# Performance work log

Hardware: AMD Instinct MI355X
Metric: run time of the kernel (lower is better)

Reference implementation:

```python
import jax, jax.numpy as jnp
import numpy as np

B, C, H, W = 4, 128, 64, 64


def setup_inputs() -> dict:
    key = jax.random.key(0)
    ks = jax.random.split(key, 7)
    s = 1.0 / np.sqrt(C)
    return {
        "x": jax.random.normal(ks[0], (B, C, H, W), dtype=jnp.float32),
        "Wq": jax.random.normal(ks[1], (C, C), dtype=jnp.float32) * s,
        "bq": jnp.zeros((C,), dtype=jnp.float32),
        "Wk": jax.random.normal(ks[2], (C, C), dtype=jnp.float32) * s,
        "bk": jnp.zeros((C,), dtype=jnp.float32),
        "Wv": jax.random.normal(ks[3], (C, C), dtype=jnp.float32) * s,
        "bv": jnp.zeros((C,), dtype=jnp.float32),
    }


def reference(x, Wq, bq, Wk, bk, Wv, bv):
    b, c, h, w = x.shape
    n = h * w
    scale = c ** (-0.5)
    # tokens: [B, N, C]
    xt = x.reshape(b, c, n).transpose(0, 2, 1)
    # 1x1 convs == per-token channel GEMMs (out[c'] = sum_c W[c',c] x[c] + b[c'])
    q = jnp.einsum("bnc,dc->bnd", xt, Wq) + bq  # [B, N, C]
    k = jnp.einsum("bnc,dc->bnd", xt, Wk) + bk  # [B, N, C]
    v = jnp.einsum("bnc,dc->bnd", xt, Wv) + bv  # [B, N, C]
    scores = jnp.einsum("bic,bjc->bij", q, k) * scale  # [B, N, N]
    attn = jax.nn.softmax(scores, axis=-1)
    out = jnp.einsum("bij,bjc->bic", attn, v)  # [B, N, C]
    return out.transpose(0, 2, 1).reshape(b, c, h, w)
```

## Files before the change

### kernel.cpp

```cpp
#include <hip/hip_runtime.h>
#include <hip/hip_bf16.h>


#define BATCH 4
#define CH    128
#define NTOK  4096
#define TK    64
#define SCALE 0.08838834764831845f
#define LOG2E 1.4426950408889634f
#define MFIX  16.0f

typedef __attribute__((ext_vector_type(8)))  short short8;
typedef __attribute__((ext_vector_type(4)))  float f32x4;
typedef __attribute__((ext_vector_type(16))) float f32x16;

static __device__ __forceinline__ unsigned short f2bf(float f) {
    __hip_bfloat16 h = (__hip_bfloat16)f;
    return *(const unsigned short*)&h;
}

static __device__ __forceinline__ unsigned cvt_pk_bf16(float lo, float hi) {
    unsigned r;
    asm("v_cvt_pk_bf16_f32 %0, %1, %2" : "=v"(r) : "v"(lo), "v"(hi));
    return r;
}

__global__ __launch_bounds__(256) void convert_w_kernel(
    const float* __restrict__ Wq, const float* __restrict__ Wk,
    const float* __restrict__ Wv, unsigned short* __restrict__ wb)
{
    const int idx = (blockIdx.x * 256 + threadIdx.x) * 4;
    const float* srcs[3] = {Wq, Wk, Wv};
    #pragma unroll
    for (int m = 0; m < 3; ++m) {
        float4 v = *(const float4*)(srcs[m] + idx);
        unsigned short o[4] = {f2bf(v.x), f2bf(v.y), f2bf(v.z), f2bf(v.w)};
        *(uint2*)(wb + (size_t)m * CH * CH + idx) = *(const uint2*)o;
    }
}

__global__ __launch_bounds__(256) void proj_mfma_kernel(
    const float* __restrict__ x,
    const unsigned short* __restrict__ wb_all,
    const float* __restrict__ bq, const float* __restrict__ bk,
    const float* __restrict__ bv,
    unsigned short* __restrict__ q_ws, unsigned short* __restrict__ k_ws,
    unsigned short* __restrict__ vt_ws)
{
    __shared__ __align__(16) unsigned short XsT[64 * CH];

    const int t    = threadIdx.x;
    const int w    = t >> 6;
    const int lane = t & 63;
    const int quad = lane >> 4;
    const int c16  = lane & 15;
    const int n0   = blockIdx.x * 64;
    const int b    = blockIdx.y;
    const int z    = blockIdx.z;
    const float* xb = x + (size_t)b * CH * NTOK;

    {
        const int tok = lane;
        #pragma unroll
        for (int cc = 0; cc < 4; ++cc) {
            const int cb = 32 * w + 8 * cc;
            unsigned short tmp[8];
            #pragma unroll
            for (int j = 0; j < 8; ++j)
                tmp[j] = f2bf(xb[(size_t)(cb + j) * NTOK + n0 + tok]);
            const int phys = ((cb >> 3) ^ (tok & 15));
            *(short8*)&XsT[tok * CH + phys * 8] = *(const short8*)tmp;
        }
    }
    __syncthreads();

    if (z < 2) {
        const unsigned short* wm = wb_all + (size_t)z * CH * CH;
        const float* bias = (z == 0) ? bq : bk;
        unsigned short* dst = (z == 0) ? q_ws : k_ws;
        const float mul = (z == 0) ? (SCALE * LOG2E) : 1.0f;

        short8 xa[4];
        #pragma unroll
        for (int ks = 0; ks < 4; ++ks)
            xa[ks] = *(const short8*)&XsT[(16 * w + c16) * CH + (((4 * ks + quad) ^ c16) << 3)];

        #pragma unroll
        for (int nt = 0; nt < 8; ++nt) {
            f32x4 a = (f32x4){0.f, 0.f, 0.f, 0.f};
            const unsigned short* wr = wm + (16 * nt + c16) * CH;
            #pragma unroll
            for (int ks = 0; ks < 4; ++ks) {
                const short8 bf = *(const short8*)(wr + 32 * ks + 8 * quad);
                a = __builtin_amdgcn_mfma_f32_16x16x32_bf16(xa[ks], bf, a, 0, 0, 0);
            }
            const float bvv = bias[16 * nt + c16];
            #pragma unroll
            for (int r = 0; r < 4; ++r) {
                const int n = n0 + 16 * w + quad * 4 + r;
                dst[((size_t)b * NTOK + n) * CH + 16 * nt + c16] =
                    f2bf((a[r] + bvv) * mul);
            }
        }
    } else {
        const unsigned short* wvb = wb_all + (size_t)2 * CH * CH;
        short8 wva[2][4];
        float  bvv[2][4];
        #pragma unroll
        for (int mt = 0; mt < 2; ++mt) {
            const int crow16 = 16 * (2 * w + mt);
            #pragma unroll
            for (int ks = 0; ks < 4; ++ks)
                wva[mt][ks] = *(const short8*)&wvb[(crow16 + c16) * CH + 32 * ks + 8 * quad];
            #pragma unroll
            for (int r = 0; r < 4; ++r)
                bvv[mt][r] = bv[crow16 + quad * 4 + r];
        }
        #pragma unroll
        for (int nt = 0; nt < 4; ++nt) {
            short8 xbf[4];
            #pragma unroll
            for (int ks = 0; ks < 4; ++ks)
                xbf[ks] = *(const short8*)&XsT[(16 * nt + c16) * CH + (((4 * ks + quad) ^ c16) << 3)];
            #pragma unroll
            for (int mt = 0; mt < 2; ++mt) {
                f32x4 acc = (f32x4){0.f, 0.f, 0.f, 0.f};
                #pragma unroll
                for (int ks = 0; ks < 4; ++ks)
                    acc = __builtin_amdgcn_mfma_f32_16x16x32_bf16(wva[mt][ks], xbf[ks], acc, 0, 0, 0);
                #pragma unroll
                for (int r = 0; r < 4; ++r) {
                    const int crow = 16 * (2 * w + mt) + quad * 4 + r;
                    vt_ws[((size_t)b * CH + crow) * NTOK + n0 + 16 * nt + c16] =
                        f2bf(acc[r] + bvv[mt][r]);
                }
            }
        }
    }
}

template <int SPLIT>
__global__ __launch_bounds__(256, 2) void flash_attn_mfma(
    const unsigned short* __restrict__ q_ws,
    const unsigned short* __restrict__ k_ws,
    const unsigned short* __restrict__ vt_ws,
    float* __restrict__ out,
    float* __restrict__ Op, float* __restrict__ l_p)
{
    __shared__ __align__(16) unsigned short KsU[2][TK * CH];
    __shared__ __align__(16) unsigned short VtU[2][CH * TK];

    const int t    = threadIdx.x;
    const int w    = t >> 6;
    const int lane = t & 63;
    const int half = lane >> 5;
    const int l32  = lane & 31;
    const int jc   = blockIdx.y;
    const int b    = blockIdx.z;
    const int n0   = blockIdx.x * 128;
    const int jbeg = jc * (NTOK / SPLIT);
    constexpr int NT = (NTOK / SPLIT) / TK;

    const unsigned short* kg = k_ws  + (size_t)b * NTOK * CH;
    const unsigned short* vg = vt_ws + (size_t)b * CH * NTOK;

    short8 qa[8];
    {
        const unsigned short* qrow =
            q_ws + ((size_t)b * NTOK + n0 + 32 * w + l32) * CH;
        #pragma unroll
        for (int ks = 0; ks < 8; ++ks)
            qa[ks] = *(const short8*)(qrow + ks * 16 + half * 8);
    }

    f32x16 Oa[4];
    #pragma unroll
    for (int ct = 0; ct < 4; ++ct) Oa[ct] = (f32x16)(0.0f);
    float lsum = 0.f;

    const int krl = lane >> 4, ku = lane & 15;
    const int vcl = lane >> 3, vu = lane & 7;

    auto STAGE = [&](int buf, int jj) {
        #pragma unroll
        for (int ci = 0; ci < 4; ++ci) {
            const int row = 16 * w + 4 * ci + krl;
            const int g   = ku ^ (row & 15);
            const unsigned short* src = kg + (size_t)(jj + row) * CH + g * 8;
            __builtin_amdgcn_global_load_lds(
                (const __attribute__((address_space(1))) void*)src,
                (__attribute__((address_space(3))) void*)&KsU[buf][(16 * w + 4 * ci) * CH],
                16, 0, 0);
        }
        #pragma unroll
        for (int ci = 0; ci < 4; ++ci) {
            const int c = 32 * w + 8 * ci + vcl;
            const int g = vu ^ (c & 7);
            const unsigned short* src = vg + (size_t)c * NTOK + jj + g * 8;
            __builtin_amdgcn_global_load_lds(
                (const __attribute__((address_space(1))) void*)src,
                (__attribute__((address_space(3))) void*)&VtU[buf][(32 * w + 8 * ci) * TK],
                16, 0, 0);
        }
    };

    STAGE(0, jbeg);

    int j0 = jbeg;
    for (int tt = 0; tt < NT; ++tt, j0 += TK) {
        const int cur = tt & 1;
        if (tt + 1 < NT) {
            STAGE(cur ^ 1, j0 + TK);
            asm volatile("s_waitcnt vmcnt(8)" ::: "memory");
        } else {
            asm volatile("s_waitcnt vmcnt(0)" ::: "memory");
        }
        __builtin_amdgcn_sched_barrier(0);
        __builtin_amdgcn_s_barrier();
        __builtin_amdgcn_sched_barrier(0);

        const unsigned short* Kc = &KsU[cur][0];
        const unsigned short* Vc = &VtU[cur][0];

        f32x16 s[2];
        s[0] = (f32x16)(-MFIX);
        s[1] = (f32x16)(-MFIX);
        #pragma unroll
        for (int ks = 0; ks < 8; ++ks) {
            const int ph = (2 * ks + half) ^ (l32 & 15);
            const short8 kf0 = *(const short8*)&Kc[l32 * CH + ph * 8];
            const short8 kf1 = *(const short8*)&Kc[(32 + l32) * CH + ph * 8];
            s[0] = __builtin_amdgcn_mfma_f32_32x32x16_bf16(kf0, qa[ks], s[0], 0, 0, 0);
            s[1] = __builtin_amdgcn_mfma_f32_32x32x16_bf16(kf1, qa[ks], s[1], 0, 0, 0);
        }

        short8 pb[4];
        #pragma unroll
        for (int kt = 0; kt < 2; ++kt) {
            float p[16];
            #pragma unroll
            for (int r = 0; r < 16; ++r) p[r] = exp2f(s[kt][r]);
            float a0 = 0.f, a1 = 0.f, a2 = 0.f, a3 = 0.f;
            #pragma unroll
            for (int r = 0; r < 4; ++r) {
                a0 += p[r]; a1 += p[4 + r]; a2 += p[8 + r]; a3 += p[12 + r];
            }
            lsum += (a0 + a1) + (a2 + a3);
            unsigned wd[8];
            #pragma unroll
            for (int i = 0; i < 8; ++i) wd[i] = cvt_pk_bf16(p[2 * i], p[2 * i + 1]);
            auto r02 = __builtin_amdgcn_permlane32_swap(wd[0], wd[2], false, false);
            auto r13 = __builtin_amdgcn_permlane32_swap(wd[1], wd[3], false, false);
            auto r46 = __builtin_amdgcn_permlane32_swap(wd[4], wd[6], false, false);
            auto r57 = __builtin_amdgcn_permlane32_swap(wd[5], wd[7], false, false);
            union { unsigned u[4]; short8 s8; } f0, f1;
            f0.u[0] = r02[0]; f0.u[1] = r13[0]; f0.u[2] = r02[1]; f0.u[3] = r13[1];
            f1.u[0] = r46[0]; f1.u[1] = r57[0]; f1.u[2] = r46[1]; f1.u[3] = r57[1];
            pb[2 * kt + 0] = f0.s8;
            pb[2 * kt + 1] = f1.s8;
        }

        #pragma unroll
        for (int ks2 = 0; ks2 < 4; ++ks2) {
            #pragma unroll
            for (int ct = 0; ct < 4; ++ct) {
                const int ch = 32 * ct + l32;
                const int ph = (2 * ks2 + half) ^ (ch & 7);
                const short8 vf = *(const short8*)&Vc[ch * TK + ph * 8];
                Oa[ct] = __builtin_amdgcn_mfma_f32_32x32x16_bf16(vf, pb[ks2], Oa[ct], 0, 0, 0);
            }
        }
        __builtin_amdgcn_sched_barrier(0);
        __builtin_amdgcn_s_barrier();
        __builtin_amdgcn_sched_barrier(0);
    }

    const float lt = lsum + __shfl_xor(lsum, 32);
    const int n = n0 + 32 * w + l32;

    if constexpr (SPLIT == 1) {
        const float inv = 1.0f / lt;
        #pragma unroll
        for (int ct = 0; ct < 4; ++ct) {
            #pragma unroll
            for (int r = 0; r < 16; ++r) {
                const int c = 32 * ct + (r & 3) + 8 * (r >> 2) + 4 * half;
                out[((size_t)b * CH + c) * NTOK + n] = Oa[ct][r] * inv;
            }
        }
    } else {
        const size_t chunk = (size_t)(b * SPLIT + jc);
        #pragma unroll
        for (int ct = 0; ct < 4; ++ct) {
            #pragma unroll
            for (int r = 0; r < 16; ++r) {
                const int c = 32 * ct + (r & 3) + 8 * (r >> 2) + 4 * half;
                Op[(chunk * CH + c) * NTOK + n] = Oa[ct][r];
            }
        }
        if (half == 0) l_p[chunk * NTOK + n] = lt;
    }
}

template <int SPLIT>
__global__ __launch_bounds__(256) void combine_kernel(
    const float* __restrict__ Op, const float* __restrict__ l_p,
    float* __restrict__ out)
{
    const int b = blockIdx.y;
    const size_t idx = ((size_t)blockIdx.x * 256 + threadIdx.x) * 4;
    const int c = (int)(idx >> 12);
    const int n = (int)(idx & (NTOK - 1));
    float4 acc = make_float4(0.f, 0.f, 0.f, 0.f);
    float4 den = make_float4(0.f, 0.f, 0.f, 0.f);
    #pragma unroll
    for (int j = 0; j < SPLIT; ++j) {
        const size_t chunk = (size_t)(b * SPLIT + j);
        const float4 o = *(const float4*)&Op[(chunk * CH + c) * NTOK + n];
        const float4 d = *(const float4*)&l_p[chunk * NTOK + n];
        acc.x += o.x; acc.y += o.y; acc.z += o.z; acc.w += o.w;
        den.x += d.x; den.y += d.y; den.z += d.z; den.w += d.w;
    }
    float4 r;
    r.x = acc.x / den.x; r.y = acc.y / den.y;
    r.z = acc.z / den.z; r.w = acc.w / den.w;
    *(float4*)&out[((size_t)b * CH * NTOK) + idx] = r;
}

extern "C" void kernel_launch(void* const* d_in, const int* in_sizes, int n_in,
                              void* d_out, int out_size, void* d_ws, size_t ws_size,
                              hipStream_t stream) {
    const float* x  = (const float*)d_in[0];
    const float* Wq = (const float*)d_in[1];
    const float* bq = (const float*)d_in[2];
    const float* Wk = (const float*)d_in[3];
    const float* bk = (const float*)d_in[4];
    const float* Wv = (const float*)d_in[5];
    const float* bv = (const float*)d_in[6];
    float* out = (float*)d_out;

    const size_t QKV = (size_t)BATCH * NTOK * CH;
    unsigned short* q_ws  = (unsigned short*)d_ws;
    unsigned short* k_ws  = q_ws + QKV;
    unsigned short* vt_ws = k_ws + QKV;
    unsigned short* wb    = vt_ws + QKV;
    float* Op = (float*)(wb + 3 * CH * CH);

    const size_t baseBytes = 3 * QKV * 2 + 3 * CH * CH * 2;
    auto needBytes = [&](size_t S) {
        return baseBytes + S * BATCH * NTOK * (size_t)(CH * 4 + 4);
    };

    convert_w_kernel<<<CH * CH / (256 * 4), 256, 0, stream>>>(Wq, Wk, Wv, wb);

    dim3 gp(NTOK / 64, BATCH, 3);
    proj_mfma_kernel<<<gp, 256, 0, stream>>>(x, wb, bq, bk, bv, q_ws, k_ws, vt_ws);

    dim3 gc(CH * NTOK / 1024, BATCH);
    if (ws_size >= needBytes(4)) {
        float* l_p = Op + (size_t)4 * BATCH * NTOK * CH;
        dim3 ga(NTOK / 128, 4, BATCH);
        flash_attn_mfma<4><<<ga, 256, 0, stream>>>(q_ws, k_ws, vt_ws, out, Op, l_p);
        combine_kernel<4><<<gc, 256, 0, stream>>>(Op, l_p, out);
    } else if (ws_size >= needBytes(2)) {
        float* l_p = Op + (size_t)2 * BATCH * NTOK * CH;
        dim3 ga(NTOK / 128, 2, BATCH);
        flash_attn_mfma<2><<<ga, 256, 0, stream>>>(q_ws, k_ws, vt_ws, out, Op, l_p);
        combine_kernel<2><<<gc, 256, 0, stream>>>(Op, l_p, out);
    } else {
        dim3 ga(NTOK / 128, 1, BATCH);
        flash_attn_mfma<1><<<ga, 256, 0, stream>>>(q_ws, k_ws, vt_ws, out,
                                                   nullptr, nullptr);
    }
}
```

Measured before the change: 132.1 us.

## Stage projection outputs through LDS for coalesced stores; raise MFMA wave priority

The projection kernel now writes its Q/K and V^T tiles into a padded shared-memory buffer and then issues 16-byte coalesced global stores, replacing scattered 2-byte stores. The attention kernel wraps its two MFMA phases in s_setprio(1) so waves doing matrix work get issue priority over waves doing exp/convert. It costs extra LDS in the projection kernel (about 18KB), which may reduce occupancy, plus an added barrier.

```diff
diff --git a/kernel.cpp b/kernel.cpp
--- a/kernel.cpp
+++ b/kernel.cpp
@@ -48,6 +48,7 @@
     unsigned short* __restrict__ vt_ws)
 {
     __shared__ __align__(16) unsigned short XsT[64 * CH];
+    __shared__ __align__(16) unsigned short Ep[128 * 72];
 
     const int t    = threadIdx.x;
     const int w    = t >> 6;
@@ -97,10 +98,17 @@
             const float bvv = bias[16 * nt + c16];
             #pragma unroll
             for (int r = 0; r < 4; ++r) {
-                const int n = n0 + 16 * w + quad * 4 + r;
-                dst[((size_t)b * NTOK + n) * CH + 16 * nt + c16] =
-                    f2bf((a[r] + bvv) * mul);
-            }
+                const int tok = 16 * w + quad * 4 + r;
+                Ep[tok * 136 + 16 * nt + c16] = f2bf((a[r] + bvv) * mul);
+            }
+        }
+        __syncthreads();
+        #pragma unroll
+        for (int p = 0; p < 4; ++p) {
+            const int tok = p * 16 + (t >> 4);
+            const int u   = t & 15;
+            const uint4 v = *(const uint4*)&Ep[tok * 136 + u * 8];
+            *(uint4*)&dst[((size_t)b * NTOK + n0 + tok) * CH + u * 8] = v;
         }
     } else {
         const unsigned short* wvb = wb_all + (size_t)2 * CH * CH;
@@ -131,10 +139,17 @@
                 #pragma unroll
                 for (int r = 0; r < 4; ++r) {
                     const int crow = 16 * (2 * w + mt) + quad * 4 + r;
-                    vt_ws[((size_t)b * CH + crow) * NTOK + n0 + 16 * nt + c16] =
-                        f2bf(acc[r] + bvv[mt][r]);
+                    Ep[crow * 72 + 16 * nt + c16] = f2bf(acc[r] + bvv[mt][r]);
                 }
             }
+        }
+        __syncthreads();
+        #pragma unroll
+        for (int p = 0; p < 4; ++p) {
+            const int c = p * 32 + (t >> 3);
+            const int u = t & 7;
+            const uint4 v = *(const uint4*)&Ep[c * 72 + u * 8];
+            *(uint4*)&vt_ws[((size_t)b * CH + c) * NTOK + n0 + u * 8] = v;
         }
     }
 }
@@ -225,6 +240,7 @@
         f32x16 s[2];
         s[0] = (f32x16)(-MFIX);
         s[1] = (f32x16)(-MFIX);
+        __builtin_amdgcn_s_setprio(1);
         #pragma unroll
         for (int ks = 0; ks < 8; ++ks) {
             const int ph = (2 * ks + half) ^ (l32 & 15);
@@ -233,6 +249,7 @@
             s[0] = __builtin_amdgcn_mfma_f32_32x32x16_bf16(kf0, qa[ks], s[0], 0, 0, 0);
             s[1] = __builtin_amdgcn_mfma_f32_32x32x16_bf16(kf1, qa[ks], s[1], 0, 0, 0);
         }
+        __builtin_amdgcn_s_setprio(0);
 
         short8 pb[4];
         #pragma unroll
@@ -260,16 +277,19 @@
             pb[2 * kt + 1] = f1.s8;
         }
 
+        __builtin_amdgcn_s_setprio(1);
         #pragma unroll
         for (int ks2 = 0; ks2 < 4; ++ks2) {
             #pragma unroll
             for (int ct = 0; ct < 4; ++ct) {
                 const int ch = 32 * ct + l32;
                 const int ph = (2 * ks2 + half) ^ (ch & 7);
-                const short8 vf = *(const short8*)&Vc[ch * TK + ph * 8];
+                const short8 vf = *(const short8*)&VtU[cur][ch * TK + ph * 8];
                 Oa[ct] = __builtin_amdgcn_mfma_f32_32x32x16_bf16(vf, pb[ks2], Oa[ct], 0, 0, 0);
             }
         }
+        __builtin_amdgcn_s_setprio(0);
+        (void)Vc;
         __builtin_amdgcn_sched_barrier(0);
         __builtin_amdgcn_s_barrier();
         __builtin_amdgcn_sched_barrier(0);
```

Result: no change. 133.7 us (+1.3%).
